# Kernel tuning notes

Hardware: AMD Instinct MI355X
Metric: run time of the kernel (lower is better)

## Reference

```python
import jax, jax.numpy as jnp
import numpy as np

D_MODEL = 256
D_CONV = 4
EXPAND = 2
D_INNER = EXPAND * D_MODEL  # 512


def silu(v):
    return v * jax.nn.sigmoid(v)


def setup_inputs() -> dict:
    key = jax.random.key(0)
    k0, k1, k2, k3, k4 = jax.random.split(key, 5)
    B, H, W = 4, 128, 128
    x = jax.random.normal(k0, (B, H, W, D_MODEL), jnp.float32)
    # nn.Linear(d_model, 2*d_inner, bias=False) -> weight (2*d_inner, d_model)
    W_in = jax.random.normal(k1, (2 * D_INNER, D_MODEL), jnp.float32) * 0.02
    # depthwise nn.Conv1d(d_inner, d_inner, k=4, groups=d_inner) -> weight (d_inner, 1, k)
    conv_w = jax.random.normal(k2, (D_INNER, 1, D_CONV), jnp.float32) * 0.1
    conv_b = jax.random.normal(k3, (D_INNER,), jnp.float32) * 0.02
    # nn.Linear(d_inner, d_model, bias=False) -> weight (d_model, d_inner)
    W_out = jax.random.normal(k4, (D_MODEL, D_INNER), jnp.float32) * 0.02
    return {"x": x, "W_in": W_in, "conv_w": conv_w, "conv_b": conv_b, "W_out": W_out}


def reference(x, W_in, conv_w, conv_b, W_out):
    B, H, W, C = x.shape
    L = H * W
    x_flat = x.reshape(B, L, C)
    xz = jnp.einsum('blc,dc->bld', x_flat, W_in)         # (B, L, 2*d_inner)
    x_branch, z_branch = jnp.split(xz, 2, axis=-1)
    # depthwise conv1d with padding=d_conv-1 then truncate to L == left-pad by d_conv-1
    u = jax.lax.conv_general_dilated(
        x_branch.transpose(0, 2, 1),                      # (B, D, L)
        conv_w,                                           # (D, 1, K)
        window_strides=(1,),
        padding=[(D_CONV - 1, 0)],
        dimension_numbers=('NCH', 'OIH', 'NCH'),
        feature_group_count=D_INNER,
    )
    u = (u + conv_b[None, :, None]).transpose(0, 2, 1)    # (B, L, D)
    u = silu(u)
    # selective_scan in the source is a stub that returns its input unchanged,
    # so the four directional passes reduce to identity transforms of u.
    y1 = u
    y2 = jnp.flip(jnp.flip(u, axis=1), axis=1)
    u_t = u.reshape(B, H, W, -1).transpose(0, 2, 1, 3).reshape(B, L, -1)
    y3 = u_t.reshape(B, W, H, -1).transpose(0, 2, 1, 3).reshape(B, L, -1)
    y4 = jnp.flip(jnp.flip(u_t, axis=1), axis=1).reshape(B, W, H, -1).transpose(0, 2, 1, 3).reshape(B, L, -1)
    y = (y1 + y2 + y3 + y4) * silu(z_branch)
    out = jnp.einsum('bld,cd->blc', y, W_out)
    return out.reshape(B, H, W, C)
```

## Files before the change

kernel.cpp:

```cpp
#include <hip/hip_runtime.h>

#define LSEQ   16384
#define BLROWS 65536
#define DM     256
#define DI     512
#define DXZ    1024

#define BM 128
#define BN 128
#define BK 32

typedef __attribute__((ext_vector_type(8))) short s16x8;
typedef __attribute__((ext_vector_type(4))) short s16x4;
typedef __attribute__((ext_vector_type(4))) float f32x4;

__device__ __forceinline__ float bf2f(unsigned short h) {
  union { unsigned u; float f; } c; c.u = ((unsigned)h) << 16; return c.f;
}
__device__ __forceinline__ unsigned short f2bf(float f) {
  union { float f; unsigned u; } c; c.f = f;
  unsigned u = c.u;
  return (unsigned short)((u + 0x7fffu + ((u >> 16) & 1u)) >> 16);
}

__global__ __launch_bounds__(256)
void cvt_f32_bf16(const float* __restrict__ src, unsigned short* __restrict__ dst, int n4) {
  for (int i = blockIdx.x * blockDim.x + threadIdx.x; i < n4; i += gridDim.x * blockDim.x) {
    const float4 v = reinterpret_cast<const float4*>(src)[i];
    s16x4 o;
    o[0] = (short)f2bf(v.x);
    o[1] = (short)f2bf(v.y);
    o[2] = (short)f2bf(v.z);
    o[3] = (short)f2bf(v.w);
    reinterpret_cast<s16x4*>(dst)[i] = o;
  }
}

__device__ __forceinline__ void gload16(const void* g, void* l) {
  __builtin_amdgcn_global_load_lds((__attribute__((address_space(1))) void*)(g),
                                   (__attribute__((address_space(3))) void*)(l),
                                   16, 0, 0);
}

__global__ __launch_bounds__(256, 4)
void gemm1_conv(const unsigned short* __restrict__ A,
                const unsigned short* __restrict__ Bw,
                const float* __restrict__ cw,
                const float* __restrict__ cb,
                unsigned short* __restrict__ Y) {
  __shared__ unsigned short lds[2][BM * BK + BN * BK];
  __shared__ float patch[2][3][64];

  const int tid  = threadIdx.x;
  const int lane = tid & 63;
  const int w    = tid >> 6;
  const int wr2  = w >> 1;
  const int wcol = w & 1;
  const int g    = lane >> 4;
  const int c0   = lane & 15;
  const int m0   = blockIdx.y * BM;
  const int n0x  = blockIdx.x * 64;

  const int srow = tid >> 2;
  const int scol = (tid & 3) * 8;

  f32x4 ax[4][2], az[4][2];
#pragma unroll
  for (int i = 0; i < 4; ++i)
#pragma unroll
    for (int j = 0; j < 2; ++j)
#pragma unroll
      for (int r = 0; r < 4; ++r) { ax[i][j][r] = 0.f; az[i][j][r] = 0.f; }

  auto stage = [&](int ks, int buf) {
    const unsigned short* Ag = A + (size_t)(m0 + srow) * DM + ks * BK + scol;
    unsigned short* lA = &lds[buf][0]       + tid * 8;
    unsigned short* lB = &lds[buf][BM * BK] + tid * 8;
#pragma unroll
    for (int i = 0; i < 2; ++i) {
      gload16(Ag + (size_t)(i * 64) * DM, lA + i * 2048);
      const int lr   = srow + i * 64;
      const int grow = (i == 0) ? (n0x + lr) : (448 + n0x + lr);
      gload16(Bw + (size_t)grow * DM + ks * BK + scol, lB + i * 2048);
    }
  };

  stage(0, 0);

  const int kSteps = DM / BK;
  for (int ks = 0; ks < kSteps; ++ks) {
    const int cur = ks & 1;
    __syncthreads();
    if (ks + 1 < kSteps) stage(ks + 1, cur ^ 1);

    const unsigned short* lA = &lds[cur][0];
    const unsigned short* lB = &lds[cur][BM * BK];
    const int lrow = lane & 15;
    const int lk   = g * 8;
    s16x8 af[4], bx[2], bz[2];
#pragma unroll
    for (int i = 0; i < 4; ++i)
      af[i] = *(const s16x8*)(lA + (wr2 * 64 + i * 16 + lrow) * BK + lk);
#pragma unroll
    for (int j = 0; j < 2; ++j) {
      bx[j] = *(const s16x8*)(lB + (wcol * 32 + j * 16 + lrow) * BK + lk);
      bz[j] = *(const s16x8*)(lB + (64 + wcol * 32 + j * 16 + lrow) * BK + lk);
    }
#pragma unroll
    for (int i = 0; i < 4; ++i)
#pragma unroll
      for (int j = 0; j < 2; ++j) {
        ax[i][j] = __builtin_amdgcn_mfma_f32_16x16x32_bf16(af[i], bx[j], ax[i][j], 0, 0, 0);
        az[i][j] = __builtin_amdgcn_mfma_f32_16x16x32_bf16(af[i], bz[j], az[i][j], 0, 0, 0);
      }
  }

  if (wr2 == 0 && g == 3) {
#pragma unroll
    for (int j = 0; j < 2; ++j) {
      const int chl = wcol * 32 + j * 16 + c0;
      patch[1][0][chl] = ax[3][j][1];
      patch[1][1][chl] = ax[3][j][2];
      patch[1][2][chl] = ax[3][j][3];
    }
  }
  if (tid < 192) {
    const int hi = tid >> 6;
    const int hc = tid & 63;
    float s = 0.f;
    if ((m0 & (LSEQ - 1)) != 0) {
      const unsigned short* xr  = A  + (size_t)(m0 - 3 + hi) * DM;
      const unsigned short* wr_ = Bw + (size_t)(n0x + hc) * DM;
#pragma unroll
      for (int kk = 0; kk < DM; kk += 8) {
        const s16x8 xa = *(const s16x8*)(xr + kk);
        const s16x8 wa = *(const s16x8*)(wr_ + kk);
#pragma unroll
        for (int jj = 0; jj < 8; ++jj)
          s += bf2f((unsigned short)xa[jj]) * bf2f((unsigned short)wa[jj]);
      }
    }
    patch[0][hi][hc] = s;
  }
  __syncthreads();

  const int src = (lane - 16) & 63;
#pragma unroll
  for (int j = 0; j < 2; ++j) {
    const int chl = wcol * 32 + j * 16 + c0;
    const int ch  = n0x + chl;
    const float4 w4 = *(const float4*)(cw + (size_t)ch * 4);
    const float cbv = cb[ch];
#pragma unroll
    for (int i = 0; i < 4; ++i) {
      const f32x4 curf = ax[i][j];
      const f32x4 prvf = (i > 0) ? ax[(i > 0 ? i - 1 : 0)][j] : ax[0][j];
      const float s1 = (g == 3) ? prvf[1] : curf[1];
      const float s2 = (g == 3) ? prvf[2] : curf[2];
      const float s3 = (g == 3) ? prvf[3] : curf[3];
      float vm3 = __shfl(s1, src);
      float vm2 = __shfl(s2, src);
      float vm1 = __shfl(s3, src);
      if (i == 0 && g == 0) {
        vm3 = patch[wr2][0][chl];
        vm2 = patch[wr2][1][chl];
        vm1 = patch[wr2][2][chl];
      }
      const float vv[7] = {vm3, vm2, vm1, curf[0], curf[1], curf[2], curf[3]};
      const int mbase = m0 + wr2 * 64 + i * 16 + g * 4;
#pragma unroll
      for (int r = 0; r < 4; ++r) {
        float a = cbv + w4.x * vv[r] + w4.y * vv[r + 1] + w4.z * vv[r + 2] + w4.w * vv[r + 3];
        const float su = a * __builtin_amdgcn_rcpf(1.f + __expf(-a));
        const float z  = az[i][j][r];
        const float sz = z * __builtin_amdgcn_rcpf(1.f + __expf(-z));
        Y[(size_t)(mbase + r) * DI + ch] = f2bf(4.f * su * sz);
      }
    }
  }
}

__global__ __launch_bounds__(256, 4)
void gemm_bt_f32(const unsigned short* __restrict__ A,
                 const unsigned short* __restrict__ B,
                 float* __restrict__ C,
                 int M, int N, int K) {
  __shared__ unsigned short lds[2][BM * BK + BN * BK];

  const int tid  = threadIdx.x;
  const int lane = tid & 63;
  const int wv   = tid >> 6;
  const int wr   = wv >> 1;
  const int wc   = wv & 1;
  const int m0   = blockIdx.y * BM;
  const int n0   = blockIdx.x * BN;

  const int srow = tid >> 2;
  const int scol = (tid & 3) * 8;

  const int kSteps = K / BK;

  f32x4 acc[4][4];
#pragma unroll
  for (int i = 0; i < 4; ++i)
#pragma unroll
    for (int j = 0; j < 4; ++j)
#pragma unroll
      for (int r = 0; r < 4; ++r) acc[i][j][r] = 0.f;

  auto stage = [&](int ks, int buf) {
    const unsigned short* Ag = A + (size_t)(m0 + srow) * K + ks * BK + scol;
    const unsigned short* Bg = B + (size_t)(n0 + srow) * K + ks * BK + scol;
    unsigned short* lA = &lds[buf][0]       + tid * 8;
    unsigned short* lB = &lds[buf][BM * BK] + tid * 8;
#pragma unroll
    for (int i = 0; i < 2; ++i) {
      gload16(Ag + (size_t)(i * 64) * K, lA + i * 2048);
      gload16(Bg + (size_t)(i * 64) * K, lB + i * 2048);
    }
  };

  stage(0, 0);

  for (int ks = 0; ks < kSteps; ++ks) {
    const int cur = ks & 1;
    __syncthreads();
    if (ks + 1 < kSteps) stage(ks + 1, cur ^ 1);

    const unsigned short* lA = &lds[cur][0];
    const unsigned short* lB = &lds[cur][BM * BK];
    const int lrow = lane & 15;
    const int lk   = (lane >> 4) * 8;
    s16x8 af[4], bf[4];
#pragma unroll
    for (int i = 0; i < 4; ++i)
      af[i] = *(const s16x8*)(lA + (wr * 64 + i * 16 + lrow) * BK + lk);
#pragma unroll
    for (int j = 0; j < 4; ++j)
      bf[j] = *(const s16x8*)(lB + (wc * 64 + j * 16 + lrow) * BK + lk);
#pragma unroll
    for (int i = 0; i < 4; ++i)
#pragma unroll
      for (int j = 0; j < 4; ++j)
        acc[i][j] = __builtin_amdgcn_mfma_f32_16x16x32_bf16(af[i], bf[j], acc[i][j], 0, 0, 0);
  }

  const int r0 = (lane >> 4) * 4;
  const int c0 = lane & 15;
#pragma unroll
  for (int i = 0; i < 4; ++i)
#pragma unroll
    for (int j = 0; j < 4; ++j) {
      const int rr = m0 + wr * 64 + i * 16 + r0;
      const int cc = n0 + wc * 64 + j * 16 + c0;
#pragma unroll
      for (int r = 0; r < 4; ++r)
        C[(size_t)(rr + r) * N + cc] = acc[i][j][r];
    }
}

extern "C" void kernel_launch(void* const* d_in, const int* in_sizes, int n_in,
                              void* d_out, int out_size, void* d_ws, size_t ws_size,
                              hipStream_t stream) {
  const float* x      = (const float*)d_in[0];
  const float* W_in   = (const float*)d_in[1];
  const float* conv_w = (const float*)d_in[2];
  const float* conv_b = (const float*)d_in[3];
  const float* W_out  = (const float*)d_in[4];

  char* ws = (char*)d_ws;
  unsigned short* y_bf    = (unsigned short*)(ws);
  unsigned short* x_bf    = (unsigned short*)(ws + (64ull << 20));
  unsigned short* win_bf  = (unsigned short*)(ws + (100ull << 20));
  unsigned short* wout_bf = (unsigned short*)(ws + (101ull << 20));

  cvt_f32_bf16<<<2048, 256, 0, stream>>>(x,     x_bf,    (BLROWS * DM) / 4);
  cvt_f32_bf16<<<256,  256, 0, stream>>>(W_in,  win_bf,  (DXZ * DM) / 4);
  cvt_f32_bf16<<<128,  256, 0, stream>>>(W_out, wout_bf, (DM * DI) / 4);

  gemm1_conv<<<dim3(DI / 64, BLROWS / BM), 256, 0, stream>>>(
      x_bf, win_bf, conv_w, conv_b, y_bf);

  gemm_bt_f32<<<dim3(DM / BN, BLROWS / BM), 256, 0, stream>>>(
      y_bf, wout_bf, (float*)d_out, BLROWS, DM, DI);
}
```

Baseline: 265.5 us.

## Replace LDS-staged output GEMM with direct global-to-register MFMA loads

The second GEMM no longer stages A and B tiles through double-buffered shared memory with barriers. Each wave now loads its MFMA fragments straight from global memory, and the K loop is fully unrolled with dimensions fixed at compile time. This removes the LDS traffic and the __syncthreads per K step. In exchange, every wave re-reads data that other waves in the block share, and the loads are strided rows rather than coalesced tiles, which relies on the cache to absorb the redundancy.

```diff
diff --git a/kernel.cpp b/kernel.cpp
--- a/kernel.cpp
+++ b/kernel.cpp
@@ -180,25 +180,19 @@
   }
 }
 
-__global__ __launch_bounds__(256, 4)
-void gemm_bt_f32(const unsigned short* __restrict__ A,
-                 const unsigned short* __restrict__ B,
-                 float* __restrict__ C,
-                 int M, int N, int K) {
-  __shared__ unsigned short lds[2][BM * BK + BN * BK];
-
+__global__ __launch_bounds__(256)
+void gemm2_direct(const unsigned short* __restrict__ A,
+                  const unsigned short* __restrict__ B,
+                  float* __restrict__ C) {
   const int tid  = threadIdx.x;
   const int lane = tid & 63;
   const int wv   = tid >> 6;
   const int wr   = wv >> 1;
   const int wc   = wv & 1;
-  const int m0   = blockIdx.y * BM;
-  const int n0   = blockIdx.x * BN;
-
-  const int srow = tid >> 2;
-  const int scol = (tid & 3) * 8;
-
-  const int kSteps = K / BK;
+  const int m0   = blockIdx.y * 128;
+  const int n0   = blockIdx.x * 128;
+  const int lrow = lane & 15;
+  const int lk0  = (lane >> 4) * 8;
 
   f32x4 acc[4][4];
 #pragma unroll
@@ -208,36 +202,22 @@
 #pragma unroll
       for (int r = 0; r < 4; ++r) acc[i][j][r] = 0.f;
 
-  auto stage = [&](int ks, int buf) {
-    const unsigned short* Ag = A + (size_t)(m0 + srow) * K + ks * BK + scol;
-    const unsigned short* Bg = B + (size_t)(n0 + srow) * K + ks * BK + scol;
-    unsigned short* lA = &lds[buf][0]       + tid * 8;
-    unsigned short* lB = &lds[buf][BM * BK] + tid * 8;
-#pragma unroll
-    for (int i = 0; i < 2; ++i) {
-      gload16(Ag + (size_t)(i * 64) * K, lA + i * 2048);
-      gload16(Bg + (size_t)(i * 64) * K, lB + i * 2048);
-    }
-  };
-
-  stage(0, 0);
-
-  for (int ks = 0; ks < kSteps; ++ks) {
-    const int cur = ks & 1;
-    __syncthreads();
-    if (ks + 1 < kSteps) stage(ks + 1, cur ^ 1);
-
-    const unsigned short* lA = &lds[cur][0];
-    const unsigned short* lB = &lds[cur][BM * BK];
-    const int lrow = lane & 15;
-    const int lk   = (lane >> 4) * 8;
+  const unsigned short* ap[4];
+  const unsigned short* bp[4];
+#pragma unroll
+  for (int i = 0; i < 4; ++i)
+    ap[i] = A + (size_t)(m0 + wr * 64 + i * 16 + lrow) * DI + lk0;
+#pragma unroll
+  for (int j = 0; j < 4; ++j)
+    bp[j] = B + (size_t)(n0 + wc * 64 + j * 16 + lrow) * DI + lk0;
+
+#pragma unroll
+  for (int ks = 0; ks < 16; ++ks) {
     s16x8 af[4], bf[4];
 #pragma unroll
-    for (int i = 0; i < 4; ++i)
-      af[i] = *(const s16x8*)(lA + (wr * 64 + i * 16 + lrow) * BK + lk);
-#pragma unroll
-    for (int j = 0; j < 4; ++j)
-      bf[j] = *(const s16x8*)(lB + (wc * 64 + j * 16 + lrow) * BK + lk);
+    for (int i = 0; i < 4; ++i) af[i] = *(const s16x8*)(ap[i] + ks * 32);
+#pragma unroll
+    for (int j = 0; j < 4; ++j) bf[j] = *(const s16x8*)(bp[j] + ks * 32);
 #pragma unroll
     for (int i = 0; i < 4; ++i)
 #pragma unroll
@@ -255,7 +235,7 @@
       const int cc = n0 + wc * 64 + j * 16 + c0;
 #pragma unroll
       for (int r = 0; r < 4; ++r)
-        C[(size_t)(rr + r) * N + cc] = acc[i][j][r];
+        C[(size_t)(rr + r) * DM + cc] = acc[i][j][r];
     }
 }
 
@@ -281,6 +261,6 @@
   gemm1_conv<<<dim3(DI / 64, BLROWS / BM), 256, 0, stream>>>(
       x_bf, win_bf, conv_w, conv_b, y_bf);
 
-  gemm_bt_f32<<<dim3(DM / BN, BLROWS / BM), 256, 0, stream>>>(
-      y_bf, wout_bf, (float*)d_out, BLROWS, DM, DI);
-}
+  gemm2_direct<<<dim3(DM / 128, BLROWS / 128), 256, 0, stream>>>(
+      y_bf, wout_bf, (float*)d_out);
+}
```

Result: slower. 296.6 us (+11.7%).

## Fuse fp32-to-bf16 conversion of x into GEMM1 A-tile staging

Applied to the files above, without the earlier changes.

Removes the standalone conversion kernel for the activation tensor and instead loads fp32 x tiles into registers, converts them to bf16, and writes them to LDS inside the first GEMM, with the next tile's loads issued before the MFMA loop and the LDS writes after it. The conv halo patch now also reads fp32 x and rounds it on the fly. This eliminates a full read/write pass over x, but each column block now reads A in fp32 (twice the bytes) instead of using async global-to-LDS loads, which adds register pressure and redundant global traffic across N-blocks.

```diff
diff --git a/kernel.cpp b/kernel.cpp
--- a/kernel.cpp
+++ b/kernel.cpp
@@ -43,7 +43,7 @@
 }
 
 __global__ __launch_bounds__(256, 4)
-void gemm1_conv(const unsigned short* __restrict__ A,
+void gemm1_conv(const float* __restrict__ X,
                 const unsigned short* __restrict__ Bw,
                 const float* __restrict__ cw,
                 const float* __restrict__ cb,
@@ -64,6 +64,9 @@
   const int srow = tid >> 2;
   const int scol = (tid & 3) * 8;
 
+  const int arow0 = tid >> 3;
+  const int ac4   = tid & 7;
+
   f32x4 ax[4][2], az[4][2];
 #pragma unroll
   for (int i = 0; i < 4; ++i)
@@ -72,26 +75,45 @@
 #pragma unroll
       for (int r = 0; r < 4; ++r) { ax[i][j][r] = 0.f; az[i][j][r] = 0.f; }
 
-  auto stage = [&](int ks, int buf) {
-    const unsigned short* Ag = A + (size_t)(m0 + srow) * DM + ks * BK + scol;
-    unsigned short* lA = &lds[buf][0]       + tid * 8;
+  float4 areg[4];
+  auto loadA = [&](int ks) {
+#pragma unroll
+    for (int i = 0; i < 4; ++i)
+      areg[i] = *(const float4*)(X + (size_t)(m0 + arow0 + i * 32) * DM + ks * BK + ac4 * 4);
+  };
+  auto writeA = [&](int buf) {
+#pragma unroll
+    for (int i = 0; i < 4; ++i) {
+      s16x4 o;
+      o[0] = (short)f2bf(areg[i].x);
+      o[1] = (short)f2bf(areg[i].y);
+      o[2] = (short)f2bf(areg[i].z);
+      o[3] = (short)f2bf(areg[i].w);
+      *(s16x4*)(&lds[buf][0] + (arow0 + i * 32) * BK + ac4 * 4) = o;
+    }
+  };
+  auto stageB = [&](int ks, int buf) {
     unsigned short* lB = &lds[buf][BM * BK] + tid * 8;
 #pragma unroll
     for (int i = 0; i < 2; ++i) {
-      gload16(Ag + (size_t)(i * 64) * DM, lA + i * 2048);
       const int lr   = srow + i * 64;
       const int grow = (i == 0) ? (n0x + lr) : (448 + n0x + lr);
       gload16(Bw + (size_t)grow * DM + ks * BK + scol, lB + i * 2048);
     }
   };
 
-  stage(0, 0);
+  loadA(0);
+  writeA(0);
+  stageB(0, 0);
 
   const int kSteps = DM / BK;
   for (int ks = 0; ks < kSteps; ++ks) {
     const int cur = ks & 1;
     __syncthreads();
-    if (ks + 1 < kSteps) stage(ks + 1, cur ^ 1);
+    if (ks + 1 < kSteps) {
+      loadA(ks + 1);
+      stageB(ks + 1, cur ^ 1);
+    }
 
     const unsigned short* lA = &lds[cur][0];
     const unsigned short* lB = &lds[cur][BM * BK];
@@ -113,6 +135,8 @@
         ax[i][j] = __builtin_amdgcn_mfma_f32_16x16x32_bf16(af[i], bx[j], ax[i][j], 0, 0, 0);
         az[i][j] = __builtin_amdgcn_mfma_f32_16x16x32_bf16(af[i], bz[j], az[i][j], 0, 0, 0);
       }
+
+    if (ks + 1 < kSteps) writeA(cur ^ 1);
   }
 
   if (wr2 == 0 && g == 3) {
@@ -129,15 +153,16 @@
     const int hc = tid & 63;
     float s = 0.f;
     if ((m0 & (LSEQ - 1)) != 0) {
-      const unsigned short* xr  = A  + (size_t)(m0 - 3 + hi) * DM;
+      const float*          xr  = X  + (size_t)(m0 - 3 + hi) * DM;
       const unsigned short* wr_ = Bw + (size_t)(n0x + hc) * DM;
 #pragma unroll
-      for (int kk = 0; kk < DM; kk += 8) {
-        const s16x8 xa = *(const s16x8*)(xr + kk);
-        const s16x8 wa = *(const s16x8*)(wr_ + kk);
-#pragma unroll
-        for (int jj = 0; jj < 8; ++jj)
-          s += bf2f((unsigned short)xa[jj]) * bf2f((unsigned short)wa[jj]);
+      for (int kk = 0; kk < DM; kk += 4) {
+        const float4 xa = *(const float4*)(xr + kk);
+        const s16x4  wa = *(const s16x4*)(wr_ + kk);
+        s += bf2f(f2bf(xa.x)) * bf2f((unsigned short)wa[0]);
+        s += bf2f(f2bf(xa.y)) * bf2f((unsigned short)wa[1]);
+        s += bf2f(f2bf(xa.z)) * bf2f((unsigned short)wa[2]);
+        s += bf2f(f2bf(xa.w)) * bf2f((unsigned short)wa[3]);
       }
     }
     patch[0][hi][hc] = s;
@@ -270,16 +295,14 @@
 
   char* ws = (char*)d_ws;
   unsigned short* y_bf    = (unsigned short*)(ws);
-  unsigned short* x_bf    = (unsigned short*)(ws + (64ull << 20));
   unsigned short* win_bf  = (unsigned short*)(ws + (100ull << 20));
   unsigned short* wout_bf = (unsigned short*)(ws + (101ull << 20));
 
-  cvt_f32_bf16<<<2048, 256, 0, stream>>>(x,     x_bf,    (BLROWS * DM) / 4);
-  cvt_f32_bf16<<<256,  256, 0, stream>>>(W_in,  win_bf,  (DXZ * DM) / 4);
-  cvt_f32_bf16<<<128,  256, 0, stream>>>(W_out, wout_bf, (DM * DI) / 4);
+  cvt_f32_bf16<<<256, 256, 0, stream>>>(W_in,  win_bf,  (DXZ * DM) / 4);
+  cvt_f32_bf16<<<128, 256, 0, stream>>>(W_out, wout_bf, (DM * DI) / 4);
 
   gemm1_conv<<<dim3(DI / 64, BLROWS / BM), 256, 0, stream>>>(
-      x_bf, win_bf, conv_w, conv_b, y_bf);
+      x, win_bf, conv_w, conv_b, y_bf);
 
   gemm_bt_f32<<<dim3(DM / BN, BLROWS / BM), 256, 0, stream>>>(
       y_bf, wout_bf, (float*)d_out, BLROWS, DM, DI);
```

Result: slower. 283.6 us (+6.8%).
